# Kernel optimization log

Measured on AMD Instinct MI355X. Metric: run time of the kernel, lower is better.

Reference implementation:

```python
import jax, jax.numpy as jnp
import numpy as np
import itertools


def setup_inputs() -> dict:
    key = jax.random.key(0)
    k1, k2 = jax.random.split(key)
    # Learned 3D LUT: [3, D, D, D], values in [0,1] like an identity/learned color LUT
    lut = jax.random.uniform(k1, (3, 33, 33, 33), dtype=jnp.float32)
    # Input RGB image batch in [0,1): [B, 3, H, W]
    x = jax.random.uniform(k2, (4, 3, 1080, 1920), dtype=jnp.float32)
    return {"lut": lut, "x": x}


def reference(lut, x):
    # Faithful JAX version of the trilinear.forward CUDA kernel:
    # per-pixel 8-corner trilinear interpolation into a [3, D, D, D] LUT.
    dim = lut.shape[-1]
    binsize = 1.000001 / (dim - 1)

    r, g, b = x[:, 0], x[:, 1], x[:, 2]  # each [B, H, W]

    inv = 1.0 / binsize
    rid = jnp.floor(r * inv).astype(jnp.int32)
    gid = jnp.floor(g * inv).astype(jnp.int32)
    bid = jnp.floor(b * inv).astype(jnp.int32)
    # fractional offsets within the cell
    fr = r * inv - rid
    fg = g * inv - gid
    fb = b * inv - bid
    # clamp so id+1 stays in range (kernel assumes x in [0,1))
    rid = jnp.clip(rid, 0, dim - 2)
    gid = jnp.clip(gid, 0, dim - 2)
    bid = jnp.clip(bid, 0, dim - 2)

    # LUT layout matches flattened index id_r + id_g*dim + id_b*dim^2
    # i.e. lut[c, b_idx, g_idx, r_idx].
    out = jnp.zeros((3,) + r.shape, dtype=x.dtype)  # [3, B, H, W]
    for db, dg, dr in itertools.product((0, 1), repeat=3):
        wr = fr if dr else (1.0 - fr)
        wg = fg if dg else (1.0 - fg)
        wb = fb if db else (1.0 - fb)
        w = wr * wg * wb  # [B, H, W]
        corner = lut[:, bid + db, gid + dg, rid + dr]  # [3, B, H, W] gather
        out = out + w[None] * corner

    return jnp.transpose(out, (1, 0, 2, 3))  # [B, 3, H, W]
```

## Files before the change

### kernel.cpp

```cpp
#include <hip/hip_runtime.h>
#include <hip/hip_fp16.h>

#define P_PLANE (1080*1920)
#define LUT_C   35937
#define N_IMG   4
#define SMEM_WORDS 35937
#define SMEM_BYTES (SMEM_WORDS * 4)

#define PPI         (P_PLANE / 8)
#define TOTAL_PAIRS (N_IMG * PPI)

typedef float fvec4 __attribute__((ext_vector_type(4)));

__global__ __launch_bounds__(256) void build_lin_u8(const float* __restrict__ lut,
                                                    unsigned int* __restrict__ T) {
    int i = blockIdx.x * blockDim.x + threadIdx.x;
    if (i >= LUT_C) return;
    unsigned int r = (unsigned int)__float2int_rn(lut[i] * 255.0f);
    unsigned int g = (unsigned int)__float2int_rn(lut[LUT_C + i] * 255.0f);
    unsigned int b = (unsigned int)__float2int_rn(lut[2 * LUT_C + i] * 255.0f);
    T[i] = r | (g << 8) | (b << 16);
}

__device__ __forceinline__ float ub0(unsigned int e) { return (float)(e & 255u); }
__device__ __forceinline__ float ub1(unsigned int e) { return (float)((e >> 8) & 255u); }
__device__ __forceinline__ float ub2(unsigned int e) { return (float)((e >> 16) & 255u); }

__global__ __launch_bounds__(1024, 4) void apply_lut_lds(const float* __restrict__ x,
                                                         const unsigned int* __restrict__ T,
                                                         float* __restrict__ out) {
    extern __shared__ unsigned int s_lut[];
    const int tid = threadIdx.x;

    {
        const uint4* Tv = (const uint4*)T;
        uint4* sv = (uint4*)s_lut;
        for (int i = tid; i < SMEM_WORDS / 4; i += blockDim.x) sv[i] = Tv[i];
        if (tid == 0) s_lut[SMEM_WORDS - 1] = T[SMEM_WORDS - 1];
    }
    __syncthreads();

    const float inv = (float)(1.0 / (1.000001 / 32.0));
    const float qs = 1.0f / 255.0f;
    const int stride = gridDim.x * blockDim.x;

    int p = blockIdx.x * blockDim.x + tid;
    if (p >= TOTAL_PAIRS) return;

    size_t base;
    {
        int n = p / PPI;
        base = (size_t)n * (3 * P_PLANE) + (size_t)(p - n * PPI) * 8;
    }
    fvec4 rA = *(const fvec4*)(x + base);
    fvec4 rB = *(const fvec4*)(x + base + 4);
    fvec4 gA = *(const fvec4*)(x + base + P_PLANE);
    fvec4 gB = *(const fvec4*)(x + base + P_PLANE + 4);
    fvec4 bA = *(const fvec4*)(x + base + 2 * P_PLANE);
    fvec4 bB = *(const fvec4*)(x + base + 2 * P_PLANE + 4);

    while (true) {
        int pn = p + stride;
        int pc = (pn < TOTAL_PAIRS) ? pn : p;
        size_t nbase;
        {
            int n = pc / PPI;
            nbase = (size_t)n * (3 * P_PLANE) + (size_t)(pc - n * PPI) * 8;
        }
        fvec4 nrA = *(const fvec4*)(x + nbase);
        fvec4 nrB = *(const fvec4*)(x + nbase + 4);
        fvec4 ngA = *(const fvec4*)(x + nbase + P_PLANE);
        fvec4 ngB = *(const fvec4*)(x + nbase + P_PLANE + 4);
        fvec4 nbA = *(const fvec4*)(x + nbase + 2 * P_PLANE);
        fvec4 nbB = *(const fvec4*)(x + nbase + 2 * P_PLANE + 4);

        int   idx[8];
        float fr[8], fg[8], fb[8];
#pragma unroll
        for (int j = 0; j < 8; ++j) {
            float r = (j < 4) ? rA[j] : rB[j - 4];
            float g = (j < 4) ? gA[j] : gB[j - 4];
            float b = (j < 4) ? bA[j] : bB[j - 4];
            float tr = r * inv, tg = g * inv, tb = b * inv;
            float fr_ = floorf(tr), fg_ = floorf(tg), fb_ = floorf(tb);
            fr[j] = tr - fr_; fg[j] = tg - fg_; fb[j] = tb - fb_;
            int ri = min(max((int)fr_, 0), 31);
            int gi = min(max((int)fg_, 0), 31);
            int bi = min(max((int)fb_, 0), 31);
            idx[j] = bi * 1089 + gi * 33 + ri;
        }

        unsigned int e[8][8];
#pragma unroll
        for (int j = 0; j < 8; ++j) {
            int i0 = idx[j];
            int i1 = idx[j] + 1089;
            e[j][0] = s_lut[i0];       e[j][1] = s_lut[i0 + 1];
            e[j][2] = s_lut[i0 + 33];  e[j][3] = s_lut[i0 + 34];
            e[j][4] = s_lut[i1];       e[j][5] = s_lut[i1 + 1];
            e[j][6] = s_lut[i1 + 33];  e[j][7] = s_lut[i1 + 34];
        }

        fvec4 oRA, oRB, oGA, oGB, oBA, oBB;
#pragma unroll
        for (int j = 0; j < 8; ++j) {
            float wr1 = fr[j], wr0 = 1.0f - fr[j];
            float wg1 = fg[j], wg0 = 1.0f - fg[j];
            float wb1 = fb[j] * qs, wb0 = (1.0f - fb[j]) * qs;
            float w00 = wb0 * wg0, w01 = wb0 * wg1, w10 = wb1 * wg0, w11 = wb1 * wg1;
            float w000 = w00 * wr0, w001 = w00 * wr1;
            float w010 = w01 * wr0, w011 = w01 * wr1;
            float w100 = w10 * wr0, w101 = w10 * wr1;
            float w110 = w11 * wr0, w111 = w11 * wr1;

            float aR = w000 * ub0(e[j][0]);
            float aG = w000 * ub1(e[j][0]);
            float aB = w000 * ub2(e[j][0]);
            aR = fmaf(w001, ub0(e[j][1]), aR); aG = fmaf(w001, ub1(e[j][1]), aG); aB = fmaf(w001, ub2(e[j][1]), aB);
            aR = fmaf(w010, ub0(e[j][2]), aR); aG = fmaf(w010, ub1(e[j][2]), aG); aB = fmaf(w010, ub2(e[j][2]), aB);
            aR = fmaf(w011, ub0(e[j][3]), aR); aG = fmaf(w011, ub1(e[j][3]), aG); aB = fmaf(w011, ub2(e[j][3]), aB);
            aR = fmaf(w100, ub0(e[j][4]), aR); aG = fmaf(w100, ub1(e[j][4]), aG); aB = fmaf(w100, ub2(e[j][4]), aB);
            aR = fmaf(w101, ub0(e[j][5]), aR); aG = fmaf(w101, ub1(e[j][5]), aG); aB = fmaf(w101, ub2(e[j][5]), aB);
            aR = fmaf(w110, ub0(e[j][6]), aR); aG = fmaf(w110, ub1(e[j][6]), aG); aB = fmaf(w110, ub2(e[j][6]), aB);
            aR = fmaf(w111, ub0(e[j][7]), aR); aG = fmaf(w111, ub1(e[j][7]), aG); aB = fmaf(w111, ub2(e[j][7]), aB);

            if (j < 4) { oRA[j] = aR;     oGA[j] = aG;     oBA[j] = aB; }
            else       { oRB[j - 4] = aR; oGB[j - 4] = aG; oBB[j - 4] = aB; }
        }

        __builtin_nontemporal_store(oRA, (fvec4*)(out + base));
        __builtin_nontemporal_store(oRB, (fvec4*)(out + base + 4));
        __builtin_nontemporal_store(oGA, (fvec4*)(out + base + P_PLANE));
        __builtin_nontemporal_store(oGB, (fvec4*)(out + base + P_PLANE + 4));
        __builtin_nontemporal_store(oBA, (fvec4*)(out + base + 2 * P_PLANE));
        __builtin_nontemporal_store(oBB, (fvec4*)(out + base + 2 * P_PLANE + 4));

        if (pn >= TOTAL_PAIRS) break;
        p = pn; base = nbase;
        rA = nrA; rB = nrB; gA = ngA; gB = ngB; bA = nbA; bB = nbB;
    }
}

__global__ __launch_bounds__(256) void build_table(const float* __restrict__ lut,
                                                   uint4* __restrict__ T) {
    int cell = blockIdx.x * blockDim.x + threadIdx.x;
    int rid = cell & 31;
    int gid = (cell >> 5) & 31;
    int bid = cell >> 10;
    const float* b0 = lut + bid * 1089 + gid * 33 + rid;
    uint4 q[4];
    __half* h = (__half*)q;
#pragma unroll
    for (int k = 0; k < 8; ++k) {
        int off = (k >> 2) * 1089 + ((k >> 1) & 1) * 33 + (k & 1);
        h[k * 4 + 0] = __float2half(b0[off]);
        h[k * 4 + 1] = __float2half(b0[LUT_C + off]);
        h[k * 4 + 2] = __float2half(b0[2 * LUT_C + off]);
        h[k * 4 + 3] = __float2half(0.0f);
    }
    uint4* dst = T + (size_t)cell * 4;
    dst[0] = q[0]; dst[1] = q[1]; dst[2] = q[2]; dst[3] = q[3];
}

__device__ __forceinline__ void acc_chunk(const uint4& q, float wA, float wB,
                                          float& aR, float& aG, float& aB) {
    const __half* h = (const __half*)&q;
    aR = fmaf(wA, __half2float(h[0]), fmaf(wB, __half2float(h[4]), aR));
    aG = fmaf(wA, __half2float(h[1]), fmaf(wB, __half2float(h[5]), aG));
    aB = fmaf(wA, __half2float(h[2]), fmaf(wB, __half2float(h[6]), aB));
}

__global__ __launch_bounds__(256) void apply_lut(const float* __restrict__ x,
                                                 const __half* __restrict__ T,
                                                 float* __restrict__ out) {
    const float inv = (float)(1.0 / (1.000001 / 32.0));
    int n  = blockIdx.y;
    int i4 = blockIdx.x * blockDim.x + threadIdx.x;
    size_t base = (size_t)n * 3 * P_PLANE + (size_t)i4 * 4;

    float4 r4 = *(const float4*)(x + base);
    float4 g4 = *(const float4*)(x + base + P_PLANE);
    float4 b4 = *(const float4*)(x + base + 2 * P_PLANE);

    float r[4] = {r4.x, r4.y, r4.z, r4.w};
    float g[4] = {g4.x, g4.y, g4.z, g4.w};
    float b[4] = {b4.x, b4.y, b4.z, b4.w};
    float oR[4], oG[4], oB[4];

#pragma unroll
    for (int i = 0; i < 4; ++i) {
        float tr = r[i] * inv;
        float tg = g[i] * inv;
        float tb = b[i] * inv;
        float fr_ = floorf(tr), fg_ = floorf(tg), fb_ = floorf(tb);
        float fr = tr - fr_, fg = tg - fg_, fb = tb - fb_;
        int ri = min(max((int)fr_, 0), 31);
        int gi = min(max((int)fg_, 0), 31);
        int bi = min(max((int)fb_, 0), 31);

        const uint4* cp = (const uint4*)(T + ((size_t)(((bi << 5) | gi) << 5 | ri) << 5));
        uint4 q0 = cp[0], q1 = cp[1], q2 = cp[2], q3 = cp[3];

        float wr1 = fr, wr0 = 1.0f - fr;
        float wg1 = fg, wg0 = 1.0f - fg;
        float wb1 = fb, wb0 = 1.0f - fb;
        float w00 = wb0 * wg0, w01 = wb0 * wg1, w10 = wb1 * wg0, w11 = wb1 * wg1;

        float aR = 0.f, aG = 0.f, aB = 0.f;
        acc_chunk(q0, w00 * wr0, w00 * wr1, aR, aG, aB);
        acc_chunk(q1, w01 * wr0, w01 * wr1, aR, aG, aB);
        acc_chunk(q2, w10 * wr0, w10 * wr1, aR, aG, aB);
        acc_chunk(q3, w11 * wr0, w11 * wr1, aR, aG, aB);

        oR[i] = aR; oG[i] = aG; oB[i] = aB;
    }

    *(float4*)(out + base)               = make_float4(oR[0], oR[1], oR[2], oR[3]);
    *(float4*)(out + base + P_PLANE)     = make_float4(oG[0], oG[1], oG[2], oG[3]);
    *(float4*)(out + base + 2 * P_PLANE) = make_float4(oB[0], oB[1], oB[2], oB[3]);
}

extern "C" void kernel_launch(void* const* d_in, const int* in_sizes, int n_in,
                              void* d_out, int out_size, void* d_ws, size_t ws_size,
                              hipStream_t stream) {
    const float* lut = (const float*)d_in[0];
    const float* x   = (const float*)d_in[1];
    float* out = (float*)d_out;

    static int max_shm = -1;
    if (max_shm < 0) {
        int dev = 0;
        (void)hipGetDevice(&dev);
        (void)hipDeviceGetAttribute(&max_shm, hipDeviceAttributeMaxSharedMemoryPerBlock, dev);
        static_assert(SMEM_BYTES == 143748, "lut lds size");
        (void)hipFuncSetAttribute((const void*)apply_lut_lds,
                                  hipFuncAttributeMaxDynamicSharedMemorySize, SMEM_BYTES);
        if (max_shm < 0) max_shm = 0;
    }

    const size_t lin_bytes = (size_t)SMEM_BYTES;
    if (max_shm >= SMEM_BYTES && ws_size >= lin_bytes) {
        unsigned int* T = (unsigned int*)d_ws;
        build_lin_u8<<<(LUT_C + 255) / 256, 256, 0, stream>>>(lut, T);
        apply_lut_lds<<<256, 1024, SMEM_BYTES, stream>>>(x, T, out);
    } else {
        __half* T = (__half*)d_ws;
        build_table<<<128, 256, 0, stream>>>(lut, (uint4*)T);
        apply_lut<<<dim3(P_PLANE / (4 * 256), N_IMG), 256, 0, stream>>>(x, T, out);
    }
}
```

Before: 205.8 us.

## Split per-thread 8-pixel work into two grid-strided quads and drop prefetch pipeline

Each thread now handles two 4-pixel groups spaced one grid-stride apart instead of 8 contiguous pixels. Adjacent lanes therefore touch adjacent 16-byte chunks, which makes the vector loads and stores contiguous across the wavefront. The software prefetch of the next iteration's inputs is removed, which cuts register pressure but gives up explicit load/compute overlap. The intent is better coalescing of global memory traffic.

```diff
diff --git a/kernel.cpp b/kernel.cpp
--- a/kernel.cpp
+++ b/kernel.cpp
@@ -6,9 +6,6 @@
 #define N_IMG   4
 #define SMEM_WORDS 35937
 #define SMEM_BYTES (SMEM_WORDS * 4)
-
-#define PPI         (P_PLANE / 8)
-#define TOTAL_PAIRS (N_IMG * PPI)
 
 typedef float fvec4 __attribute__((ext_vector_type(4)));
 
@@ -42,37 +39,26 @@
 
     const float inv = (float)(1.0 / (1.000001 / 32.0));
     const float qs = 1.0f / 255.0f;
-    const int stride = gridDim.x * blockDim.x;
-
-    int p = blockIdx.x * blockDim.x + tid;
-    if (p >= TOTAL_PAIRS) return;
-
-    size_t base;
-    {
-        int n = p / PPI;
-        base = (size_t)n * (3 * P_PLANE) + (size_t)(p - n * PPI) * 8;
-    }
-    fvec4 rA = *(const fvec4*)(x + base);
-    fvec4 rB = *(const fvec4*)(x + base + 4);
-    fvec4 gA = *(const fvec4*)(x + base + P_PLANE);
-    fvec4 gB = *(const fvec4*)(x + base + P_PLANE + 4);
-    fvec4 bA = *(const fvec4*)(x + base + 2 * P_PLANE);
-    fvec4 bB = *(const fvec4*)(x + base + 2 * P_PLANE + 4);
-
-    while (true) {
-        int pn = p + stride;
-        int pc = (pn < TOTAL_PAIRS) ? pn : p;
-        size_t nbase;
-        {
-            int n = pc / PPI;
-            nbase = (size_t)n * (3 * P_PLANE) + (size_t)(pc - n * PPI) * 8;
-        }
-        fvec4 nrA = *(const fvec4*)(x + nbase);
-        fvec4 nrB = *(const fvec4*)(x + nbase + 4);
-        fvec4 ngA = *(const fvec4*)(x + nbase + P_PLANE);
-        fvec4 ngB = *(const fvec4*)(x + nbase + P_PLANE + 4);
-        fvec4 nbA = *(const fvec4*)(x + nbase + 2 * P_PLANE);
-        fvec4 nbB = *(const fvec4*)(x + nbase + 2 * P_PLANE + 4);
+    const int QPI = P_PLANE / 4;
+    const int total = N_IMG * QPI;
+    const int G = gridDim.x * blockDim.x;
+
+    for (int q0 = blockIdx.x * blockDim.x + tid; q0 < total; q0 += 2 * G) {
+        int q1 = q0 + G;
+        const bool has2 = (q1 < total);
+        int q1c = has2 ? q1 : q0;
+
+        int n0 = q0 / QPI;
+        size_t base0 = (size_t)n0 * (3 * P_PLANE) + (size_t)(q0 - n0 * QPI) * 4;
+        int n1 = q1c / QPI;
+        size_t base1 = (size_t)n1 * (3 * P_PLANE) + (size_t)(q1c - n1 * QPI) * 4;
+
+        fvec4 rA = *(const fvec4*)(x + base0);
+        fvec4 gA = *(const fvec4*)(x + base0 + P_PLANE);
+        fvec4 bA = *(const fvec4*)(x + base0 + 2 * P_PLANE);
+        fvec4 rB = *(const fvec4*)(x + base1);
+        fvec4 gB = *(const fvec4*)(x + base1 + P_PLANE);
+        fvec4 bB = *(const fvec4*)(x + base1 + 2 * P_PLANE);
 
         int   idx[8];
         float fr[8], fg[8], fb[8];
@@ -101,7 +87,7 @@
             e[j][6] = s_lut[i1 + 33];  e[j][7] = s_lut[i1 + 34];
         }
 
-        fvec4 oRA, oRB, oGA, oGB, oBA, oBB;
+        fvec4 oRA, oGA, oBA, oRB, oGB, oBB;
 #pragma unroll
         for (int j = 0; j < 8; ++j) {
             float wr1 = fr[j], wr0 = 1.0f - fr[j];
@@ -128,16 +114,14 @@
             else       { oRB[j - 4] = aR; oGB[j - 4] = aG; oBB[j - 4] = aB; }
         }
 
-        __builtin_nontemporal_store(oRA, (fvec4*)(out + base));
-        __builtin_nontemporal_store(oRB, (fvec4*)(out + base + 4));
-        __builtin_nontemporal_store(oGA, (fvec4*)(out + base + P_PLANE));
-        __builtin_nontemporal_store(oGB, (fvec4*)(out + base + P_PLANE + 4));
-        __builtin_nontemporal_store(oBA, (fvec4*)(out + base + 2 * P_PLANE));
-        __builtin_nontemporal_store(oBB, (fvec4*)(out + base + 2 * P_PLANE + 4));
-
-        if (pn >= TOTAL_PAIRS) break;
-        p = pn; base = nbase;
-        rA = nrA; rB = nrB; gA = ngA; gB = ngB; bA = nbA; bB = nbB;
+        __builtin_nontemporal_store(oRA, (fvec4*)(out + base0));
+        __builtin_nontemporal_store(oGA, (fvec4*)(out + base0 + P_PLANE));
+        __builtin_nontemporal_store(oBA, (fvec4*)(out + base0 + 2 * P_PLANE));
+        if (has2) {
+            __builtin_nontemporal_store(oRB, (fvec4*)(out + base1));
+            __builtin_nontemporal_store(oGB, (fvec4*)(out + base1 + P_PLANE));
+            __builtin_nontemporal_store(oBB, (fvec4*)(out + base1 + 2 * P_PLANE));
+        }
     }
 }
 
```

Measured after the change: 185.3 us. 1.11x faster.
